# Kernel tuning notes

Hardware: AMD Instinct MI355X
Metric: run time of the kernel (lower is better)

Reference implementation:

```python
import jax, jax.numpy as jnp
import numpy as np

D_MODEL = 1024
N_HEADS = 16
D_K = D_MODEL // N_HEADS
RANK = 16
LORA_SCALING = 32.0 / RANK  # alpha / rank = 2.0
LN_EPS = 1e-5


def _lora_linear(x, w, b, A, B):
    # torch nn.Linear: x @ w.T + b ; LoRA: (x @ A @ B) * scaling
    return x @ w.T + b + (x @ A @ B) * LORA_SCALING


def setup_inputs() -> dict:
    key = jax.random.key(0)
    ks = jax.random.split(key, 20)
    d = {}
    d['x'] = jax.random.normal(ks[0], (4, 1024, D_MODEL), dtype=jnp.float32)
    i = 1
    for p in ('q', 'k', 'v', 'o'):
        d[f'{p}_w'] = jax.random.normal(ks[i], (D_MODEL, D_MODEL), dtype=jnp.float32) * (1.0 / np.sqrt(D_MODEL)); i += 1
        d[f'{p}_b'] = jax.random.normal(ks[i], (D_MODEL,), dtype=jnp.float32) * 0.01; i += 1
        d[f'{p}_A'] = jax.random.normal(ks[i], (D_MODEL, RANK), dtype=jnp.float32) * 0.01; i += 1
        d[f'{p}_B'] = jax.random.normal(ks[i], (RANK, D_MODEL), dtype=jnp.float32) * 0.01; i += 1
    d['ln_g'] = jnp.ones((D_MODEL,), dtype=jnp.float32)
    d['ln_b'] = jnp.zeros((D_MODEL,), dtype=jnp.float32)
    return d


def reference(x, q_w, q_b, q_A, q_B, k_w, k_b, k_A, k_B,
              v_w, v_b, v_A, v_B, o_w, o_b, o_A, o_B, ln_g, ln_b):
    B, S, _ = x.shape
    # QKV projections with LoRA, reshape to [B, H, S, d_k]
    def split_heads(t):
        return t.reshape(B, S, N_HEADS, D_K).transpose(0, 2, 1, 3)
    Q = split_heads(_lora_linear(x, q_w, q_b, q_A, q_B))
    K = split_heads(_lora_linear(x, k_w, k_b, k_A, k_B))
    V = split_heads(_lora_linear(x, v_w, v_b, v_A, v_B))

    scores = jnp.einsum('bhqd,bhkd->bhqk', Q, K) / jnp.sqrt(jnp.float32(D_K))
    attn = jax.nn.softmax(scores, axis=-1)  # dropout is identity in eval
    ctx = jnp.einsum('bhqk,bhkd->bhqd', attn, V)
    ctx = ctx.transpose(0, 2, 1, 3).reshape(B, S, D_MODEL)

    out = _lora_linear(ctx, o_w, o_b, o_A, o_B)
    # residual + LayerNorm
    h = out + x
    mu = jnp.mean(h, axis=-1, keepdims=True)
    var = jnp.mean(jnp.square(h - mu), axis=-1, keepdims=True)
    normed = (h - mu) * jax.lax.rsqrt(var + LN_EPS) * ln_g + ln_b
    return normed, attn.mean(axis=1)
```

## Files before the change

### kernel.cpp

```cpp
#include <hip/hip_runtime.h>

#define DMODEL 1024
#define NHEADS 16
#define DHEAD  64
#define RANK   16
#define BATCH  4
#define SEQ    1024
#define MTOT   (BATCH*SEQ)
#define QSCALE 0.18033688011112042f

typedef __bf16 bf16;
typedef __bf16 bf16x8 __attribute__((ext_vector_type(8)));
typedef __bf16 bf16x4 __attribute__((ext_vector_type(4)));
typedef float  f32x4  __attribute__((ext_vector_type(4)));

__device__ __forceinline__ int swz128(int row, int byte_in_row) {
  int slot = byte_in_row >> 4;
  return row * 128 + (((slot ^ (row & 7)) << 4) | (byte_in_row & 15));
}

__device__ __forceinline__ void gll16(const void* g, void* l) {
  __builtin_amdgcn_global_load_lds((const __attribute__((address_space(1))) unsigned int*)g,
                                   (__attribute__((address_space(3))) unsigned int*)l, 16, 0, 0);
}

#define TRRD(lo, hi, base, o0, o1)                                   \
  asm volatile("ds_read_b64_tr_b16 %0, %2 offset:" #o0 "\n\t"        \
               "ds_read_b64_tr_b16 %1, %2 offset:" #o1               \
               : "=v"(lo), "=v"(hi) : "v"(base));

__global__ void prep_weff_kernel(
    const float* __restrict__ W0, const float* __restrict__ A0, const float* __restrict__ B0,
    const float* __restrict__ W1, const float* __restrict__ A1, const float* __restrict__ B1,
    const float* __restrict__ W2, const float* __restrict__ A2, const float* __restrict__ B2,
    const float* __restrict__ W3, const float* __restrict__ A3, const float* __restrict__ B3,
    bf16* __restrict__ out) {
  const int l = blockIdx.y;
  const float* W = l == 0 ? W0 : l == 1 ? W1 : l == 2 ? W2 : W3;
  const float* A = l == 0 ? A0 : l == 1 ? A1 : l == 2 ? A2 : A3;
  const float* Bm = l == 0 ? B0 : l == 1 ? B1 : l == 2 ? B2 : B3;
  out += (size_t)l * DMODEL * DMODEL;
  const int n = blockIdx.x;
  __shared__ float bsc[RANK];
  if (threadIdx.x < RANK) bsc[threadIdx.x] = Bm[threadIdx.x * DMODEL + n] * 2.0f;
  __syncthreads();
  float br[RANK];
#pragma unroll
  for (int r = 0; r < RANK; ++r) br[r] = bsc[r];
  for (int k0 = 0; k0 < DMODEL; k0 += 256) {
    int k = k0 + threadIdx.x;
    float acc = W[n * DMODEL + k];
    const float4* arow = (const float4*)(A + k * RANK);
#pragma unroll
    for (int r4 = 0; r4 < 4; ++r4) {
      float4 a = arow[r4];
      acc += a.x*br[r4*4+0] + a.y*br[r4*4+1] + a.z*br[r4*4+2] + a.w*br[r4*4+3];
    }
    out[n * DMODEL + k] = (bf16)acc;
  }
}

__global__ void cast_x_kernel(const float* __restrict__ x, bf16* __restrict__ xb) {
  int i = (blockIdx.x * blockDim.x + threadIdx.x) * 4;
  float4 v = *(const float4*)(x + i);
  bf16x4 o = { (bf16)v.x, (bf16)v.y, (bf16)v.z, (bf16)v.w };
  *(bf16x4*)(xb + i) = o;
}

__device__ __forceinline__ void gemm_core64(
    const bf16* __restrict__ Ain, const bf16* __restrict__ Bin,
    char* sA, char* sB, int m0, int n0, f32x4 (&acc)[2][4]) {
  const int tid = threadIdx.x;
  const int w = tid >> 6, lane = tid & 63;
  const int wm = (w & 1) * 32, wn = (w >> 1) * 64;
  const bf16* pA[2]; char* lA[2];
  const bf16* pB[4]; char* lB[4];
#pragma unroll
  for (int i = 0; i < 2; ++i) {
    int chunk = i * 4 + w;
    int row = chunk * 8 + (lane >> 3);
    int ss = (lane & 7) ^ (row & 7);
    pA[i] = Ain + (size_t)(m0 + row) * DMODEL + ss * 8;
    lA[i] = sA + chunk * 1024;
  }
#pragma unroll
  for (int i = 0; i < 4; ++i) {
    int chunk = i * 4 + w;
    int row = chunk * 8 + (lane >> 3);
    int ss = (lane & 7) ^ (row & 7);
    pB[i] = Bin + (size_t)(n0 + row) * DMODEL + ss * 8;
    lB[i] = sB + chunk * 1024;
  }
  for (int kt = 0; kt < DMODEL / 64; ++kt) {
    const int kbase = kt * 64;
#pragma unroll
    for (int i = 0; i < 2; ++i) gll16(pA[i] + kbase, lA[i]);
#pragma unroll
    for (int i = 0; i < 4; ++i) gll16(pB[i] + kbase, lB[i]);
    __syncthreads();
#pragma unroll
    for (int ks = 0; ks < 2; ++ks) {
      bf16x8 af[2], bfg[4];
#pragma unroll
      for (int mi = 0; mi < 2; ++mi)
        af[mi] = *(const bf16x8*)(sA + swz128(wm + mi*16 + (lane & 15), ks*64 + (lane >> 4)*16));
#pragma unroll
      for (int ni = 0; ni < 4; ++ni)
        bfg[ni] = *(const bf16x8*)(sB + swz128(wn + ni*16 + (lane & 15), ks*64 + (lane >> 4)*16));
#pragma unroll
      for (int mi = 0; mi < 2; ++mi)
#pragma unroll
        for (int ni = 0; ni < 4; ++ni)
          acc[mi][ni] = __builtin_amdgcn_mfma_f32_16x16x32_bf16(af[mi], bfg[ni], acc[mi][ni], 0, 0, 0);
    }
    __syncthreads();
  }
}

__global__ __launch_bounds__(256) void gemm_qkv_kernel(
    const bf16* __restrict__ xb, const bf16* __restrict__ weff,
    const float* __restrict__ bq, const float* __restrict__ bk, const float* __restrict__ bv,
    bf16* __restrict__ Qb, bf16* __restrict__ Kb, bf16* __restrict__ Vb)
{
  __shared__ __align__(16) char sA[8192];
  __shared__ __align__(16) char sB[16384];
  const int tid = threadIdx.x, w = tid >> 6, lane = tid & 63;
  const int bid = blockIdx.x;
  const int nb = (bid & 7) * 192 + (bid >> 3);
  const int n0 = (nb % 24) * 128, m0 = (nb / 24) * 64;
  const int z = n0 >> 10;
  const float* bias = z == 0 ? bq : z == 1 ? bk : bv;
  bf16* outp = z == 0 ? Qb : (z == 1 ? Kb : Vb);
  const float scl = z == 0 ? QSCALE : 1.0f;
  const int wm = (w & 1) * 32, wn = (w >> 1) * 64;
  f32x4 acc[2][4] = {};
  gemm_core64(xb, weff, sA, sB, m0, n0, acc);
#pragma unroll
  for (int mi = 0; mi < 2; ++mi) {
#pragma unroll
    for (int ni = 0; ni < 4; ++ni) {
      int col = n0 + wn + ni * 16 + (lane & 15);
      float bcol = bias[col & 1023];
      int h = (col >> 6) & 15, d = col & 63;
#pragma unroll
      for (int r = 0; r < 4; ++r) {
        int row = m0 + wm + mi * 16 + (lane >> 4) * 4 + r;
        float v = (acc[mi][ni][r] + bcol) * scl;
        int b = row >> 10, s = row & 1023;
        outp[(size_t)((b * NHEADS + h) * SEQ + s) * DHEAD + d] = (bf16)v;
      }
    }
  }
}

__global__ __launch_bounds__(256) void gemm_o_kernel(
    const bf16* __restrict__ ctx, const bf16* __restrict__ weff,
    const float* __restrict__ bias, const float* __restrict__ resid,
    float* __restrict__ outf)
{
  __shared__ __align__(16) char sA[8192];
  __shared__ __align__(16) char sB[16384];
  const int tid = threadIdx.x, w = tid >> 6, lane = tid & 63;
  const int bid = blockIdx.x;
  const int nb = (bid & 7) * 64 + (bid >> 3);
  const int n0 = (nb & 7) * 128, m0 = (nb >> 3) * 64;
  const int wm = (w & 1) * 32, wn = (w >> 1) * 64;
  f32x4 acc[2][4] = {};
  gemm_core64(ctx, weff, sA, sB, m0, n0, acc);
#pragma unroll
  for (int mi = 0; mi < 2; ++mi) {
#pragma unroll
    for (int ni = 0; ni < 4; ++ni) {
      int col = n0 + wn + ni * 16 + (lane & 15);
      float bcol = bias[col];
#pragma unroll
      for (int r = 0; r < 4; ++r) {
        int row = m0 + wm + mi * 16 + (lane >> 4) * 4 + r;
        outf[(size_t)row * DMODEL + col] =
            acc[mi][ni][r] + bcol + resid[(size_t)row * DMODEL + col];
      }
    }
  }
}

__global__ __launch_bounds__(256) void flash_kernel(
    const bf16* __restrict__ Qb, const bf16* __restrict__ Kb, const bf16* __restrict__ Vb,
    bf16* __restrict__ ctx, float* __restrict__ lstat)
{
  __shared__ __align__(16) char sK[64 * 128];
  __shared__ __align__(16) char sV[8192];
  __shared__ __align__(16) char sP[4 * 2048];
  const int tid = threadIdx.x, w = tid >> 6, lane = tid & 63;
  const int bid = blockIdx.x;
  const int nb = (bid & 7) * 128 + (bid >> 3);
  const int bh = nb >> 4;
  const int q0 = (nb & 15) * 64;
  const bf16* Qbase = Qb + (size_t)bh * SEQ * DHEAD;
  const bf16* Kbase = Kb + (size_t)bh * SEQ * DHEAD;
  const bf16* Vbase = Vb + (size_t)bh * SEQ * DHEAD;
  const int qw = q0 + w * 16;

  bf16x8 aq[2];
#pragma unroll
  for (int ks = 0; ks < 2; ++ks)
    aq[ks] = *(const bf16x8*)(Qbase + (size_t)(qw + (lane & 15)) * DHEAD + ks * 32 + (lane >> 4) * 8);

  const bf16* pK[2]; const bf16* pV[2]; char* lK[2]; char* lV[2];
#pragma unroll
  for (int i = 0; i < 2; ++i) {
    int ci = i * 4 + w;
    int rowK = ci * 8 + (lane >> 3);
    int ssK = (lane & 7) ^ (rowK & 7);
    pK[i] = Kbase + (size_t)rowK * DHEAD + ssK * 8;
    lK[i] = sK + ci * 1024;
    int kV = ci * 8 + ((lane >> 5) & 1) * 4 + ((lane >> 1) & 3);
    int dV = (((lane >> 3) & 3) << 4) + ((lane & 1) << 3);
    pV[i] = Vbase + (size_t)kV * DHEAD + dV;
    lV[i] = sV + ci * 1024;
  }

  char* sPw = sP + w * 2048;
  const unsigned pbase = (unsigned)(uintptr_t)sPw + ((lane >> 4) << 8) + ((lane & 15) << 3);
  const unsigned vbase0 = (unsigned)(uintptr_t)sV + ((lane >> 4) << 10) + ((lane & 15) << 3);
  char* pwr = sPw + ((lane >> 4) << 3) + (lane & 15) * 32;

  f32x4 cacc[4] = {};
  float lsum[4] = {0.f, 0.f, 0.f, 0.f};

  for (int kt = 0; kt < SEQ / 64; ++kt) {
    const size_t kofs = (size_t)(kt * 64) * DHEAD;
#pragma unroll
    for (int i = 0; i < 2; ++i) {
      gll16(pK[i] + kofs, lK[i]);
      gll16(pV[i] + kofs, lV[i]);
    }
    __syncthreads();

    f32x4 sc[4] = {};
#pragma unroll
    for (int ks = 0; ks < 2; ++ks)
#pragma unroll
      for (int ni = 0; ni < 4; ++ni) {
        bf16x8 bk = *(const bf16x8*)(sK + swz128(ni*16 + (lane & 15), ks*64 + (lane >> 4)*16));
        sc[ni] = __builtin_amdgcn_mfma_f32_16x16x32_bf16(aq[ks], bk, sc[ni], 0, 0, 0);
      }

#pragma unroll
    for (int ni = 0; ni < 4; ++ni) {
      float p0 = __builtin_amdgcn_exp2f(sc[ni][0]);
      float p1 = __builtin_amdgcn_exp2f(sc[ni][1]);
      float p2 = __builtin_amdgcn_exp2f(sc[ni][2]);
      float p3 = __builtin_amdgcn_exp2f(sc[ni][3]);
      lsum[0] += p0; lsum[1] += p1; lsum[2] += p2; lsum[3] += p3;
      bf16x4 pb = { (bf16)p0, (bf16)p1, (bf16)p2, (bf16)p3 };
      *(bf16x4*)(pwr + ni * 512) = pb;
    }
    asm volatile("s_waitcnt lgkmcnt(0)" ::: "memory");

    unsigned long long t0, t1, v0[4], v1[4];
    TRRD(t0, t1, pbase, 0, 128)
    TRRD(v0[0], v1[0], vbase0, 0, 512)
    TRRD(v0[1], v1[1], vbase0, 128, 640)
    TRRD(v0[2], v1[2], vbase0, 256, 768)
    TRRD(v0[3], v1[3], vbase0, 384, 896)
    asm volatile("s_waitcnt lgkmcnt(0)" ::: "memory");
    __builtin_amdgcn_sched_barrier(0);
    {
      union { unsigned long long u[2]; bf16x8 v; } pu, vu;
      pu.u[0] = t0; pu.u[1] = t1;
#pragma unroll
      for (int ni = 0; ni < 4; ++ni) {
        vu.u[0] = v0[ni]; vu.u[1] = v1[ni];
        cacc[ni] = __builtin_amdgcn_mfma_f32_16x16x32_bf16(pu.v, vu.v, cacc[ni], 0, 0, 0);
      }
    }
    TRRD(t0, t1, pbase, 1024, 1152)
    TRRD(v0[0], v1[0], vbase0, 4096, 4608)
    TRRD(v0[1], v1[1], vbase0, 4224, 4736)
    TRRD(v0[2], v1[2], vbase0, 4352, 4864)
    TRRD(v0[3], v1[3], vbase0, 4480, 4992)
    asm volatile("s_waitcnt lgkmcnt(0)" ::: "memory");
    __builtin_amdgcn_sched_barrier(0);
    {
      union { unsigned long long u[2]; bf16x8 v; } pu, vu;
      pu.u[0] = t0; pu.u[1] = t1;
#pragma unroll
      for (int ni = 0; ni < 4; ++ni) {
        vu.u[0] = v0[ni]; vu.u[1] = v1[ni];
        cacc[ni] = __builtin_amdgcn_mfma_f32_16x16x32_bf16(pu.v, vu.v, cacc[ni], 0, 0, 0);
      }
    }
    __syncthreads();
  }

#pragma unroll
  for (int r = 0; r < 4; ++r) {
#pragma unroll
    for (int off = 1; off < 16; off <<= 1) lsum[r] += __shfl_xor(lsum[r], off);
  }

  const int b = bh >> 4, hh = bh & 15;
#pragma unroll
  for (int r = 0; r < 4; ++r) {
    float inv = __builtin_amdgcn_rcpf(lsum[r]);
    int qrow = qw + (lane >> 4) * 4 + r;
#pragma unroll
    for (int ni = 0; ni < 4; ++ni) {
      int d = ni * 16 + (lane & 15);
      ctx[(size_t)(b * SEQ + qrow) * DMODEL + hh * DHEAD + d] = (bf16)(cacc[ni][r] * inv);
    }
    if ((lane & 15) == 0) lstat[(size_t)bh * SEQ + qrow] = lsum[r];
  }
}

__global__ __launch_bounds__(256) void mean_kernel(
    const bf16* __restrict__ Qb, const bf16* __restrict__ Kb,
    const float* __restrict__ lstat, float* __restrict__ out2)
{
  __shared__ __align__(16) char sK[2 * 16384];
  const int tid = threadIdx.x, w = tid >> 6, lane = tid & 63;
  const int bid = blockIdx.x;
  const int nb2 = (bid & 7) * 64 + (bid >> 3);
  const int b = nb2 >> 7;
  const int q0 = ((nb2 >> 3) & 15) * 64, k0 = (nb2 & 7) * 128;
  const int qw = q0 + w * 16;
  size_t goff[4]; int lofs[4];
#pragma unroll
  for (int i = 0; i < 4; ++i) {
    int chunk = i * 4 + w;
    int row = chunk * 8 + (lane >> 3);
    int ss = (lane & 7) ^ (row & 7);
    goff[i] = (size_t)(k0 + row) * DHEAD + ss * 8;
    lofs[i] = chunk * 1024;
  }
  const bf16* Kb_b = Kb + (size_t)b * NHEADS * SEQ * DHEAD;
  const bf16* Qb_b = Qb + (size_t)b * NHEADS * SEQ * DHEAD;

  f32x4 macc[8] = {};
#pragma unroll
  for (int i = 0; i < 4; ++i) gll16(Kb_b + goff[i], sK + lofs[i]);
  asm volatile("s_waitcnt vmcnt(0)" ::: "memory");
  __syncthreads();

  for (int h = 0; h < NHEADS; ++h) {
    const int cur = (h & 1) << 14, nxt = cur ^ 16384;
    if (h + 1 < NHEADS) {
      const bf16* Kn = Kb_b + (size_t)(h + 1) * SEQ * DHEAD;
#pragma unroll
      for (int i = 0; i < 4; ++i) gll16(Kn + goff[i], sK + nxt + lofs[i]);
    }
    const bf16* Qbase = Qb_b + (size_t)h * SEQ * DHEAD;
    bf16x8 aq[2];
#pragma unroll
    for (int ks = 0; ks < 2; ++ks)
      aq[ks] = *(const bf16x8*)(Qbase + (size_t)(qw + (lane & 15)) * DHEAD
                                + ks * 32 + (lane >> 4) * 8);
    char* cK = sK + cur;
    f32x4 sc[8] = {};
#pragma unroll
    for (int ks = 0; ks < 2; ++ks)
#pragma unroll
      for (int ni = 0; ni < 8; ++ni) {
        bf16x8 bk = *(const bf16x8*)(cK + swz128(ni*16 + (lane & 15), ks*64 + (lane >> 4)*16));
        sc[ni] = __builtin_amdgcn_mfma_f32_16x16x32_bf16(aq[ks], bk, sc[ni], 0, 0, 0);
      }
    float lsc[4];
    const float* ls = lstat + ((size_t)(b * NHEADS + h)) * SEQ;
#pragma unroll
    for (int r = 0; r < 4; ++r)
      lsc[r] = 0.0625f * __builtin_amdgcn_rcpf(ls[qw + (lane >> 4)*4 + r]);
#pragma unroll
    for (int ni = 0; ni < 8; ++ni)
#pragma unroll
      for (int r = 0; r < 4; ++r)
        macc[ni][r] += __builtin_amdgcn_exp2f(sc[ni][r]) * lsc[r];
    asm volatile("s_waitcnt vmcnt(0)" ::: "memory");
    __syncthreads();
  }
#pragma unroll
  for (int r = 0; r < 4; ++r) {
    int qrow = qw + (lane >> 4) * 4 + r;
#pragma unroll
    for (int ni = 0; ni < 8; ++ni)
      out2[(size_t)(b * SEQ + qrow) * SEQ + k0 + ni * 16 + (lane & 15)] = macc[ni][r];
  }
}

__global__ __launch_bounds__(256) void ln_kernel(
    float* __restrict__ hb, const float* __restrict__ g,
    const float* __restrict__ bvec, float* __restrict__ out)
{
  const int row = blockIdx.x, t = threadIdx.x;
  float4 v = *(const float4*)(hb + (size_t)row * DMODEL + t * 4);
  float s = v.x + v.y + v.z + v.w;
  float s2 = v.x*v.x + v.y*v.y + v.z*v.z + v.w*v.w;
#pragma unroll
  for (int off = 32; off >= 1; off >>= 1) {
    s  += __shfl_down(s, off);
    s2 += __shfl_down(s2, off);
  }
  __shared__ float red[8];
  const int w = t >> 6;
  if ((t & 63) == 0) { red[w] = s; red[4 + w] = s2; }
  __syncthreads();
  if (t == 0) {
    red[0] = red[0] + red[1] + red[2] + red[3];
    red[4] = red[4] + red[5] + red[6] + red[7];
  }
  __syncthreads();
  float mu = red[0] * (1.0f / DMODEL);
  float var = red[4] * (1.0f / DMODEL) - mu * mu;
  float rs = rsqrtf(var + 1e-5f);
  float4 gv = *(const float4*)(g + t * 4);
  float4 bv = *(const float4*)(bvec + t * 4);
  float4 o;
  o.x = (v.x - mu) * rs * gv.x + bv.x;
  o.y = (v.y - mu) * rs * gv.y + bv.y;
  o.z = (v.z - mu) * rs * gv.z + bv.z;
  o.w = (v.w - mu) * rs * gv.w + bv.w;
  *(float4*)(out + (size_t)row * DMODEL + t * 4) = o;
}

extern "C" void kernel_launch(void* const* d_in, const int* in_sizes, int n_in,
                              void* d_out, int out_size, void* d_ws, size_t ws_size,
                              hipStream_t stream) {
  (void)in_sizes; (void)n_in; (void)out_size; (void)ws_size;
  const float* x = (const float*)d_in[0];
  const float* w_[4]  = {(const float*)d_in[1],  (const float*)d_in[5],
                         (const float*)d_in[9],  (const float*)d_in[13]};
  const float* b_[4]  = {(const float*)d_in[2],  (const float*)d_in[6],
                         (const float*)d_in[10], (const float*)d_in[14]};
  const float* A_[4]  = {(const float*)d_in[3],  (const float*)d_in[7],
                         (const float*)d_in[11], (const float*)d_in[15]};
  const float* Bm_[4] = {(const float*)d_in[4],  (const float*)d_in[8],
                         (const float*)d_in[12], (const float*)d_in[16]};
  const float* lng = (const float*)d_in[17];
  const float* lnb = (const float*)d_in[18];

  char* ws = (char*)d_ws;
  bf16* xb    = (bf16*)(ws);
  bf16* weff  = (bf16*)(ws + (8u  << 20));
  bf16* Qb    = (bf16*)(ws + (16u << 20));
  bf16* Kb    = (bf16*)(ws + (24u << 20));
  bf16* Vb    = (bf16*)(ws + (32u << 20));
  float* lstat = (float*)(ws + (40u << 20));
  bf16* ctx = xb;
  float* hbuf = (float*)d_out;
  float* out2 = (float*)d_out + (size_t)MTOT * DMODEL;

  prep_weff_kernel<<<dim3(DMODEL, 4), dim3(256), 0, stream>>>(
      w_[0], A_[0], Bm_[0], w_[1], A_[1], Bm_[1],
      w_[2], A_[2], Bm_[2], w_[3], A_[3], Bm_[3], weff);
  cast_x_kernel<<<dim3(MTOT * DMODEL / 1024), dim3(256), 0, stream>>>(x, xb);

  gemm_qkv_kernel<<<dim3(1536), 256, 0, stream>>>(
      xb, weff, b_[0], b_[1], b_[2], Qb, Kb, Vb);

  flash_kernel<<<dim3(1024), 256, 0, stream>>>(Qb, Kb, Vb, ctx, lstat);
  mean_kernel<<<dim3(512), 256, 0, stream>>>(Qb, Kb, lstat, out2);
  gemm_o_kernel<<<dim3(512), 256, 0, stream>>>(
      ctx, weff + 3u * DMODEL * DMODEL, b_[3], x, hbuf);
  ln_kernel<<<dim3(MTOT), 256, 0, stream>>>(hbuf, lng, lnb, hbuf);
}
```

Measured before the change: 146.9 us.

## Double-buffer K/V tiles and pass P through ds_bpermute instead of LDS

The flash attention kernel now double-buffers the K and V tiles in shared memory, prefetching the next tile while computing on the current one, and drops the per-iteration wait before compute. The QK^T MFMA operands are swapped so each lane holds a transposed score layout. The probability matrix is then packed to bf16 and reshuffled into A-operand layout with ds_bpermute, replacing the write-to-LDS-then-transpose-read round trip. The row-sum reduction is simplified to match. This adds LDS footprint, which may lower occupancy, and adds cross-lane permute instructions.

```diff
diff --git a/kernel.cpp b/kernel.cpp
--- a/kernel.cpp
+++ b/kernel.cpp
@@ -22,6 +22,12 @@
 __device__ __forceinline__ void gll16(const void* g, void* l) {
   __builtin_amdgcn_global_load_lds((const __attribute__((address_space(1))) unsigned int*)g,
                                    (__attribute__((address_space(3))) unsigned int*)l, 16, 0, 0);
+}
+
+__device__ __forceinline__ unsigned pack2(float a, float b) {
+  union { bf16 h[2]; unsigned u; } x;
+  x.h[0] = (bf16)a; x.h[1] = (bf16)b;
+  return x.u;
 }
 
 #define TRRD(lo, hi, base, o0, o1)                                   \
@@ -187,9 +193,8 @@
     const bf16* __restrict__ Qb, const bf16* __restrict__ Kb, const bf16* __restrict__ Vb,
     bf16* __restrict__ ctx, float* __restrict__ lstat)
 {
-  __shared__ __align__(16) char sK[64 * 128];
-  __shared__ __align__(16) char sV[8192];
-  __shared__ __align__(16) char sP[4 * 2048];
+  __shared__ __align__(16) char sK[2 * 8192];
+  __shared__ __align__(16) char sV[2 * 8192];
   const int tid = threadIdx.x, w = tid >> 6, lane = tid & 63;
   const int bid = blockIdx.x;
   const int nb = (bid & 7) * 128 + (bid >> 3);
@@ -205,111 +210,120 @@
   for (int ks = 0; ks < 2; ++ks)
     aq[ks] = *(const bf16x8*)(Qbase + (size_t)(qw + (lane & 15)) * DHEAD + ks * 32 + (lane >> 4) * 8);
 
-  const bf16* pK[2]; const bf16* pV[2]; char* lK[2]; char* lV[2];
+  const bf16* pK[2]; const bf16* pV[2]; int lKo[2]; int lVo[2];
 #pragma unroll
   for (int i = 0; i < 2; ++i) {
     int ci = i * 4 + w;
     int rowK = ci * 8 + (lane >> 3);
     int ssK = (lane & 7) ^ (rowK & 7);
     pK[i] = Kbase + (size_t)rowK * DHEAD + ssK * 8;
-    lK[i] = sK + ci * 1024;
+    lKo[i] = ci * 1024;
     int kV = ci * 8 + ((lane >> 5) & 1) * 4 + ((lane >> 1) & 3);
     int dV = (((lane >> 3) & 3) << 4) + ((lane & 1) << 3);
     pV[i] = Vbase + (size_t)kV * DHEAD + dV;
-    lV[i] = sV + ci * 1024;
-  }
-
-  char* sPw = sP + w * 2048;
-  const unsigned pbase = (unsigned)(uintptr_t)sPw + ((lane >> 4) << 8) + ((lane & 15) << 3);
+    lVo[i] = ci * 1024;
+  }
+
   const unsigned vbase0 = (unsigned)(uintptr_t)sV + ((lane >> 4) << 10) + ((lane & 15) << 3);
-  char* pwr = sPw + ((lane >> 4) << 3) + (lane & 15) * 32;
+  const int addr0 = 4 * ((lane & 15) + 32 * ((lane >> 4) & 1));
+  const int addr1 = addr0 + 64;
+  const bool hi5 = (lane & 32) != 0;
 
   f32x4 cacc[4] = {};
-  float lsum[4] = {0.f, 0.f, 0.f, 0.f};
+  float lsum = 0.f;
+
+#pragma unroll
+  for (int i = 0; i < 2; ++i) {
+    gll16(pK[i], sK + lKo[i]);
+    gll16(pV[i], sV + lVo[i]);
+  }
+  asm volatile("s_waitcnt vmcnt(0)" ::: "memory");
+  __syncthreads();
 
   for (int kt = 0; kt < SEQ / 64; ++kt) {
-    const size_t kofs = (size_t)(kt * 64) * DHEAD;
-#pragma unroll
-    for (int i = 0; i < 2; ++i) {
-      gll16(pK[i] + kofs, lK[i]);
-      gll16(pV[i] + kofs, lV[i]);
-    }
-    __syncthreads();
-
+    const int cur = (kt & 1) << 13, nxt = cur ^ 8192;
+    if (kt + 1 < SEQ / 64) {
+      const size_t kofs = (size_t)((kt + 1) * 64) * DHEAD;
+#pragma unroll
+      for (int i = 0; i < 2; ++i) {
+        gll16(pK[i] + kofs, sK + nxt + lKo[i]);
+        gll16(pV[i] + kofs, sV + nxt + lVo[i]);
+      }
+    }
     f32x4 sc[4] = {};
 #pragma unroll
     for (int ks = 0; ks < 2; ++ks)
 #pragma unroll
       for (int ni = 0; ni < 4; ++ni) {
-        bf16x8 bk = *(const bf16x8*)(sK + swz128(ni*16 + (lane & 15), ks*64 + (lane >> 4)*16));
-        sc[ni] = __builtin_amdgcn_mfma_f32_16x16x32_bf16(aq[ks], bk, sc[ni], 0, 0, 0);
-      }
-
+        bf16x8 bk = *(const bf16x8*)(sK + cur + swz128(ni*16 + (lane & 15), ks*64 + (lane >> 4)*16));
+        sc[ni] = __builtin_amdgcn_mfma_f32_16x16x32_bf16(bk, aq[ks], sc[ni], 0, 0, 0);
+      }
+    unsigned long long v0[2][4], v1[2][4];
+    const unsigned vb = vbase0 + cur;
+    TRRD(v0[0][0], v1[0][0], vb, 0, 512)
+    TRRD(v0[0][1], v1[0][1], vb, 128, 640)
+    TRRD(v0[0][2], v1[0][2], vb, 256, 768)
+    TRRD(v0[0][3], v1[0][3], vb, 384, 896)
+    TRRD(v0[1][0], v1[1][0], vb, 4096, 4608)
+    TRRD(v0[1][1], v1[1][1], vb, 4224, 4736)
+    TRRD(v0[1][2], v1[1][2], vb, 4352, 4864)
+    TRRD(v0[1][3], v1[1][3], vb, 4480, 4992)
+    unsigned P2[4][2];
 #pragma unroll
     for (int ni = 0; ni < 4; ++ni) {
-      float p0 = __builtin_amdgcn_exp2f(sc[ni][0]);
-      float p1 = __builtin_amdgcn_exp2f(sc[ni][1]);
-      float p2 = __builtin_amdgcn_exp2f(sc[ni][2]);
-      float p3 = __builtin_amdgcn_exp2f(sc[ni][3]);
-      lsum[0] += p0; lsum[1] += p1; lsum[2] += p2; lsum[3] += p3;
-      bf16x4 pb = { (bf16)p0, (bf16)p1, (bf16)p2, (bf16)p3 };
-      *(bf16x4*)(pwr + ni * 512) = pb;
-    }
-    asm volatile("s_waitcnt lgkmcnt(0)" ::: "memory");
-
-    unsigned long long t0, t1, v0[4], v1[4];
-    TRRD(t0, t1, pbase, 0, 128)
-    TRRD(v0[0], v1[0], vbase0, 0, 512)
-    TRRD(v0[1], v1[1], vbase0, 128, 640)
-    TRRD(v0[2], v1[2], vbase0, 256, 768)
-    TRRD(v0[3], v1[3], vbase0, 384, 896)
+      float e0 = __builtin_amdgcn_exp2f(sc[ni][0]);
+      float e1 = __builtin_amdgcn_exp2f(sc[ni][1]);
+      float e2 = __builtin_amdgcn_exp2f(sc[ni][2]);
+      float e3 = __builtin_amdgcn_exp2f(sc[ni][3]);
+      lsum += (e0 + e1) + (e2 + e3);
+      P2[ni][0] = pack2(e0, e1);
+      P2[ni][1] = pack2(e2, e3);
+    }
+    unsigned pa[2][4];
+#pragma unroll
+    for (int ks = 0; ks < 2; ++ks)
+#pragma unroll
+      for (int t = 0; t < 4; ++t) {
+        int ad = (t >> 1) ? addr1 : addr0;
+        int lo = __builtin_amdgcn_ds_bpermute(ad, (int)P2[2*ks][t & 1]);
+        int hi = __builtin_amdgcn_ds_bpermute(ad, (int)P2[2*ks + 1][t & 1]);
+        pa[ks][t] = hi5 ? (unsigned)hi : (unsigned)lo;
+      }
     asm volatile("s_waitcnt lgkmcnt(0)" ::: "memory");
     __builtin_amdgcn_sched_barrier(0);
-    {
-      union { unsigned long long u[2]; bf16x8 v; } pu, vu;
-      pu.u[0] = t0; pu.u[1] = t1;
+#pragma unroll
+    for (int ks = 0; ks < 2; ++ks) {
+      union { unsigned u[4]; bf16x8 v; } A;
+      A.u[0] = pa[ks][0]; A.u[1] = pa[ks][1]; A.u[2] = pa[ks][2]; A.u[3] = pa[ks][3];
 #pragma unroll
       for (int ni = 0; ni < 4; ++ni) {
-        vu.u[0] = v0[ni]; vu.u[1] = v1[ni];
-        cacc[ni] = __builtin_amdgcn_mfma_f32_16x16x32_bf16(pu.v, vu.v, cacc[ni], 0, 0, 0);
-      }
-    }
-    TRRD(t0, t1, pbase, 1024, 1152)
-    TRRD(v0[0], v1[0], vbase0, 4096, 4608)
-    TRRD(v0[1], v1[1], vbase0, 4224, 4736)
-    TRRD(v0[2], v1[2], vbase0, 4352, 4864)
-    TRRD(v0[3], v1[3], vbase0, 4480, 4992)
-    asm volatile("s_waitcnt lgkmcnt(0)" ::: "memory");
-    __builtin_amdgcn_sched_barrier(0);
-    {
-      union { unsigned long long u[2]; bf16x8 v; } pu, vu;
-      pu.u[0] = t0; pu.u[1] = t1;
-#pragma unroll
-      for (int ni = 0; ni < 4; ++ni) {
-        vu.u[0] = v0[ni]; vu.u[1] = v1[ni];
-        cacc[ni] = __builtin_amdgcn_mfma_f32_16x16x32_bf16(pu.v, vu.v, cacc[ni], 0, 0, 0);
-      }
-    }
+        union { unsigned long long u[2]; bf16x8 v; } V;
+        V.u[0] = v0[ks][ni]; V.u[1] = v1[ks][ni];
+        cacc[ni] = __builtin_amdgcn_mfma_f32_16x16x32_bf16(A.v, V.v, cacc[ni], 0, 0, 0);
+      }
+    }
+    asm volatile("s_waitcnt vmcnt(0)" ::: "memory");
     __syncthreads();
   }
 
+  lsum += __shfl_xor(lsum, 16);
+  lsum += __shfl_xor(lsum, 32);
+  float lq[4];
+#pragma unroll
+  for (int r = 0; r < 4; ++r)
+    lq[r] = __shfl(lsum, 4 * (lane >> 4) + r);
+
+  const int b = bh >> 4, hh = bh & 15;
 #pragma unroll
   for (int r = 0; r < 4; ++r) {
-#pragma unroll
-    for (int off = 1; off < 16; off <<= 1) lsum[r] += __shfl_xor(lsum[r], off);
-  }
-
-  const int b = bh >> 4, hh = bh & 15;
-#pragma unroll
-  for (int r = 0; r < 4; ++r) {
-    float inv = __builtin_amdgcn_rcpf(lsum[r]);
+    float inv = __builtin_amdgcn_rcpf(lq[r]);
     int qrow = qw + (lane >> 4) * 4 + r;
 #pragma unroll
     for (int ni = 0; ni < 4; ++ni) {
       int d = ni * 16 + (lane & 15);
       ctx[(size_t)(b * SEQ + qrow) * DMODEL + hh * DHEAD + d] = (bf16)(cacc[ni][r] * inv);
     }
-    if ((lane & 15) == 0) lstat[(size_t)bh * SEQ + qrow] = lsum[r];
+    if ((lane & 15) == 0) lstat[(size_t)bh * SEQ + qrow] = lq[r];
   }
 }
 
```

Result: slower. 154.4 us (+5.1%).
